# Optimization experiments

Hardware: AMD Instinct MI355X
Metric: run time of the kernel (lower is better)

## Reference

```python
import jax, jax.numpy as jnp
import numpy as np

GROUPS = 32
EPS = 1e-6


def group_norm(h, scale, bias):
    B, C, H, W = h.shape
    hg = h.reshape(B, GROUPS, -1)
    mu = hg.mean(axis=-1, keepdims=True)
    var = hg.var(axis=-1, keepdims=True)
    hg = (hg - mu) * jax.lax.rsqrt(var + EPS)
    h = hg.reshape(B, C, H, W)
    return h * scale[None, :, None, None] + bias[None, :, None, None]


def conv1x1(h, W, b):
    # 1x1 conv == per-pixel linear: (B,C,H,W) x (O,C) -> (B,O,H,W)
    return jnp.einsum('bchw,oc->bohw', h, W) + b[None, :, None, None]


def setup_inputs() -> dict:
    key = jax.random.key(0)
    ks = jax.random.split(key, 6)
    B, C, H, W = 8, 512, 64, 64
    s = 0.02
    return {
        'x': jax.random.normal(ks[0], (B, C, H, W), jnp.float32),
        'gn_scale': jnp.ones((C,), jnp.float32),
        'gn_bias': jnp.zeros((C,), jnp.float32),
        'Wq': jax.random.normal(ks[1], (C, C), jnp.float32) * s,
        'bq': jnp.zeros((C,), jnp.float32),
        'Wk': jax.random.normal(ks[2], (C, C), jnp.float32) * s,
        'bk': jnp.zeros((C,), jnp.float32),
        'Wv': jax.random.normal(ks[3], (C, C), jnp.float32) * s,
        'bv': jnp.zeros((C,), jnp.float32),
        'Wo': jax.random.normal(ks[4], (C, C), jnp.float32) * s,
        'bo': jnp.zeros((C,), jnp.float32),
    }


def reference(x, gn_scale, gn_bias, Wq, bq, Wk, bk, Wv, bv, Wo, bo):
    B, C, H, W = x.shape
    N = H * W
    h = group_norm(x, gn_scale, gn_bias)
    q = conv1x1(h, Wq, bq).reshape(B, C, N)   # (B,C,N)
    k = conv1x1(h, Wk, bk).reshape(B, C, N)
    v = conv1x1(h, Wv, bv).reshape(B, C, N)
    # scores: q^T k, scaled by C^-0.5
    w = jnp.einsum('bcq,bck->bqk', q, k) * (C ** -0.5)  # (B,N_q,N_k)
    w = jax.nn.softmax(w, axis=-1)
    # h = v @ w^T  -> (B,C,N_q)
    h = jnp.einsum('bck,bqk->bcq', v, w).reshape(B, C, H, W)
    h = conv1x1(h, Wo, bo)
    return x + h
```

## Files before the change

kernel.cpp:

```cpp
#include <hip/hip_runtime.h>
#include <math.h>

typedef __bf16 bf16_t;
typedef __bf16 bf8v __attribute__((ext_vector_type(8)));
typedef __bf16 bf4v __attribute__((ext_vector_type(4)));
typedef float  f4v  __attribute__((ext_vector_type(4)));

#define BB  8
#define CC  512
#define NN  4096
#define CPG 16
#define NCb (NN * CC)
#define WSZ (CC * CC)

#define FLG_SIZES 805306368.f
#define FLG_WS    536870912.f

__global__ void diag_out(float* out, float v) { if (threadIdx.x == 0) out[0] = v; }

__device__ __forceinline__ void gload_lds16(const bf16_t* g, bf16_t* l)
{
    __builtin_amdgcn_global_load_lds(
        (const __attribute__((address_space(1))) unsigned int*)g,
        (__attribute__((address_space(3))) unsigned int*)l, 16, 0, 0);
}

__global__ __launch_bounds__(256) void cvt_w(const float* __restrict__ a,
                                             const float* __restrict__ b,
                                             const float* __restrict__ c,
                                             const float* __restrict__ d,
                                             bf16_t* __restrict__ o)
{
    const int i = (blockIdx.x * 256 + threadIdx.x) * 4;
    const float* srcs[4] = {a, b, c, d};
#pragma unroll
    for (int m = 0; m < 4; m++) {
        float4 v = *(const float4*)(srcs[m] + i);
        bf4v w;
        w[0] = (bf16_t)v.x; w[1] = (bf16_t)v.y;
        w[2] = (bf16_t)v.z; w[3] = (bf16_t)v.w;
        *(bf4v*)(o + (size_t)m * WSZ + i) = w;
    }
}

__global__ __launch_bounds__(256) void gn_stats_part(const float* __restrict__ x,
                                                     double* __restrict__ part)
{
    const int bg = blockIdx.x >> 2;
    const int sl = blockIdx.x & 3;
    const int tid = threadIdx.x;
    const float4* xv = (const float4*)(x + (size_t)bg * CPG * NN) + sl * 4096;
    double s[4] = {0, 0, 0, 0}, ss[4] = {0, 0, 0, 0};
#pragma unroll
    for (int ii = 0; ii < 16; ii++) {
        float4 v = xv[tid + ii * 256];
        const int a = ii & 3;
        s[a]  += (double)v.x + (double)v.y + (double)v.z + (double)v.w;
        ss[a] += (double)v.x * v.x + (double)v.y * v.y
               + (double)v.z * v.z + (double)v.w * v.w;
    }
    double sT = s[0] + s[1] + s[2] + s[3];
    double ssT = ss[0] + ss[1] + ss[2] + ss[3];
    __shared__ double l1[256], l2[256];
    l1[tid] = sT; l2[tid] = ssT;
    __syncthreads();
    for (int o = 128; o > 0; o >>= 1) {
        if (tid < o) { l1[tid] += l1[tid + o]; l2[tid] += l2[tid + o]; }
        __syncthreads();
    }
    if (tid == 0) {
        part[(size_t)blockIdx.x * 2]     = l1[0];
        part[(size_t)blockIdx.x * 2 + 1] = l2[0];
    }
}

__global__ __launch_bounds__(256) void gn_stats_fin(const double* __restrict__ part,
                                                    float* __restrict__ stats)
{
    const int bg = threadIdx.x;
    double s = 0.0, ss = 0.0;
#pragma unroll
    for (int sl = 0; sl < 4; sl++) {
        s  += part[(size_t)(bg * 4 + sl) * 2];
        ss += part[(size_t)(bg * 4 + sl) * 2 + 1];
    }
    double mean = s * (1.0 / 65536.0);
    double var  = ss * (1.0 / 65536.0) - mean * mean;
    stats[bg * 2]     = (float)mean;
    stats[bg * 2 + 1] = (float)(1.0 / sqrt(var + 1e-6));
}

__global__ __launch_bounds__(256) void gn_apply_all(const float* __restrict__ x,
                                                    const float* __restrict__ gw,
                                                    const float* __restrict__ gb,
                                                    const float* __restrict__ stats,
                                                    bf16_t* __restrict__ h_all)
{
    const int b  = blockIdx.y;
    const int g  = blockIdx.x >> 4;
    const int sl = blockIdx.x & 15;
    const float* xp = x + (size_t)b * CC * NN + (size_t)g * CPG * NN;
    bf16_t* h = h_all + (size_t)b * NCb;
    const int tid = threadIdx.x;
    const float mean = stats[(b * 32 + g) * 2];
    const float rstd = stats[(b * 32 + g) * 2 + 1];
    const int cw = tid & 15;
    const float aa = rstd * gw[g * CPG + cw];
    const float bb = gb[g * CPG + cw] - mean * aa;

    __shared__ float tile[CPG][260];
    const int n0 = sl * 256;
    for (int i = tid; i < (CPG * 256) / 4; i += 256) {
        int c  = i >> 6;
        int n4 = i & 63;
        float4 v = *(const float4*)(xp + (size_t)c * NN + n0 + n4 * 4);
        tile[c][n4 * 4 + 0] = v.x;
        tile[c][n4 * 4 + 1] = v.y;
        tile[c][n4 * 4 + 2] = v.z;
        tile[c][n4 * 4 + 3] = v.w;
    }
    __syncthreads();
#pragma unroll
    for (int j = 0; j < 16; j++) {
        int n = (tid >> 4) + 16 * j;
        float v = tile[cw][n] * aa + bb;
        h[(size_t)(n0 + n) * CC + g * CPG + cw] = (bf16_t)v;
    }
}

__global__ __launch_bounds__(256) void gn_apply(const float* __restrict__ xb,
                                                const float* __restrict__ gw,
                                                const float* __restrict__ gb,
                                                const float* __restrict__ stats,
                                                bf16_t* __restrict__ h,
                                                int bg0)
{
    const int g  = blockIdx.x >> 4;
    const int sl = blockIdx.x & 15;
    const float* xp = xb + (size_t)g * CPG * NN;
    const int tid = threadIdx.x;
    const float mean = stats[(bg0 + g) * 2];
    const float rstd = stats[(bg0 + g) * 2 + 1];
    const int cw = tid & 15;
    const float aa = rstd * gw[g * CPG + cw];
    const float bb = gb[g * CPG + cw] - mean * aa;

    __shared__ float tile[CPG][260];
    const int n0 = sl * 256;
    for (int i = tid; i < (CPG * 256) / 4; i += 256) {
        int c  = i >> 6;
        int n4 = i & 63;
        float4 v = *(const float4*)(xp + (size_t)c * NN + n0 + n4 * 4);
        tile[c][n4 * 4 + 0] = v.x;
        tile[c][n4 * 4 + 1] = v.y;
        tile[c][n4 * 4 + 2] = v.z;
        tile[c][n4 * 4 + 3] = v.w;
    }
    __syncthreads();
#pragma unroll
    for (int j = 0; j < 16; j++) {
        int n = (tid >> 4) + 16 * j;
        float v = tile[cw][n] * aa + bb;
        h[(size_t)(n0 + n) * CC + g * CPG + cw] = (bf16_t)v;
    }
}

#define ABUF (128 * 32)
#define BBUF (256 * 32)
#define NBUF 3

__device__ __forceinline__ void stage_tile(
    const bf16_t* pa, const bf16_t* pb, int lda, int ldb,
    bf16_t* lA, bf16_t* lB)
{
    gload_lds16(pa,                     lA);
    gload_lds16(pa + (size_t)16 * lda,  lA + 16 * 32);
    gload_lds16(pb,                     lB);
    gload_lds16(pb + (size_t)16 * ldb,  lB + 16 * 32);
    gload_lds16(pb + (size_t)32 * ldb,  lB + 32 * 32);
    gload_lds16(pb + (size_t)48 * ldb,  lB + 48 * 32);
}

__device__ __forceinline__ void gemm_core_w(
    const bf16_t* __restrict__ A, const bf16_t* __restrict__ B,
    int K, int lda, int ldb, size_t m0, size_t n0,
    bf16_t* Asm, bf16_t* Bsm,
    int wave, int lane, int wm, int wn, int fr, int fq, f4v acc[4][8])
{
    const int gr  = lane >> 2;
    const int gcs = (((lane & 3) ^ (gr & 3)) << 3);
    const bf16_t* pa = A + (m0 + wave * 32 + gr) * lda + gcs;
    const bf16_t* pb = B + (n0 + wave * 64 + gr) * ldb + gcs;
    const int la0 = (wave * 32) * 32;
    const int lb0 = (wave * 64) * 32;
    const int fqs = ((fq ^ (fr & 3)) << 3);

    stage_tile(pa, pb, lda, ldb, Asm + la0, Bsm + lb0);
    if (K > 32)
        stage_tile(pa + 32, pb + 32, lda, ldb,
                   Asm + ABUF + la0, Bsm + BBUF + lb0);

    int buf = 0;
    for (int kt = 0; kt < K; kt += 32) {
        if (kt + 64 < K) {
            const int nb = (buf + 2 >= NBUF) ? buf + 2 - NBUF : buf + 2;
            stage_tile(pa + kt + 64, pb + kt + 64, lda, ldb,
                       Asm + nb * ABUF + la0, Bsm + nb * BBUF + lb0);
            asm volatile("s_waitcnt vmcnt(12)" ::: "memory");
        } else if (kt + 32 < K) {
            asm volatile("s_waitcnt vmcnt(6)" ::: "memory");
        } else {
            asm volatile("s_waitcnt vmcnt(0)" ::: "memory");
        }
        __builtin_amdgcn_s_barrier();

        const bf16_t* As = Asm + buf * ABUF;
        const bf16_t* Bs = Bsm + buf * BBUF;
        bf8v af[4], bfv[8];
#pragma unroll
        for (int j = 0; j < 8; j++)
            bfv[j] = *(const bf8v*)(Bs + (wn + j * 16 + fr) * 32 + fqs);
#pragma unroll
        for (int i = 0; i < 4; i++)
            af[i] = *(const bf8v*)(As + (wm + i * 16 + fr) * 32 + fqs);
#pragma unroll
        for (int i = 0; i < 4; i++)
#pragma unroll
            for (int j = 0; j < 8; j++)
                acc[i][j] = __builtin_amdgcn_mfma_f32_16x16x32_bf16(
                    af[i], bfv[j], acc[i][j], 0, 0, 0);

        __builtin_amdgcn_s_barrier();
        buf = (buf + 1 == NBUF) ? 0 : buf + 1;
    }
}

template <int MODE>
__global__ __launch_bounds__(256, 2) void gemm_bt(
    const bf16_t* __restrict__ A, const bf16_t* __restrict__ B,
    void* __restrict__ Og, const float* __restrict__ bias,
    const float* __restrict__ resid, float scale,
    int K, int lda, int ldb, int ldo)
{
    __shared__ bf16_t Asm[NBUF * ABUF];
    __shared__ bf16_t Bsm[NBUF * BBUF];
    const int tid  = threadIdx.x;
    const int lane = tid & 63, wave = tid >> 6;
    const int wm = (wave >> 1) << 6, wn = (wave & 1) << 7;
    const int fr = lane & 15, fq = lane >> 4;
    const size_t m0 = (size_t)blockIdx.x * 128, n0 = (size_t)blockIdx.y * 256;

    f4v acc[4][8];
#pragma unroll
    for (int i = 0; i < 4; i++)
#pragma unroll
        for (int j = 0; j < 8; j++) acc[i][j] = (f4v){0.f, 0.f, 0.f, 0.f};

    gemm_core_w(A, B, K, lda, ldb, m0, n0, Asm, Bsm,
                wave, lane, wm, wn, fr, fq, acc);

    if (MODE == 0) {
        bf16_t* out = (bf16_t*)Og;
#pragma unroll
        for (int i = 0; i < 4; i++) {
            const int mb = (int)m0 + wm + i * 16 + fq * 4;
#pragma unroll
            for (int j = 0; j < 8; j++) {
                const int n = (int)n0 + wn + j * 16 + fr;
                const float bn = bias ? bias[n] : 0.f;
#pragma unroll
                for (int t = 0; t < 4; t++)
                    out[(size_t)(mb + t) * ldo + n] =
                        (bf16_t)(acc[i][j][t] * scale + bn);
            }
        }
    } else {
        float* out = (float*)Og;
#pragma unroll
        for (int i = 0; i < 4; i++) {
            const int mb = (int)m0 + wm + i * 16 + fq * 4;
#pragma unroll
            for (int j = 0; j < 8; j++) {
                const int n = (int)n0 + wn + j * 16 + fr;
                const float bn = bias[n];
                float4 rq = *(const float4*)(resid + (size_t)n * ldo + mb);
                float4 o4;
                o4.x = acc[i][j][0] * scale + bn + rq.x;
                o4.y = acc[i][j][1] * scale + bn + rq.y;
                o4.z = acc[i][j][2] * scale + bn + rq.z;
                o4.w = acc[i][j][3] * scale + bn + rq.w;
                *(float4*)(out + (size_t)n * ldo + mb) = o4;
            }
        }
    }
}

__global__ __launch_bounds__(256, 2) void gemm_qkv(
    const bf16_t* __restrict__ h, const bf16_t* __restrict__ Wb,
    const float* __restrict__ bq, const float* __restrict__ bk,
    const float* __restrict__ bv,
    bf16_t* __restrict__ q, bf16_t* __restrict__ k, bf16_t* __restrict__ v)
{
    __shared__ bf16_t Asm[NBUF * ABUF];
    __shared__ bf16_t Bsm[NBUF * BBUF];
    const int z = blockIdx.z;
    const bf16_t* B = Wb + (size_t)z * WSZ;
    const float* bias = (z == 0) ? bq : (z == 1) ? bk : bv;
    bf16_t* out = (z == 0) ? q : (z == 1) ? k : v;

    const int tid  = threadIdx.x;
    const int lane = tid & 63, wave = tid >> 6;
    const int wm = (wave >> 1) << 6, wn = (wave & 1) << 7;
    const int fr = lane & 15, fq = lane >> 4;
    const size_t m0 = (size_t)blockIdx.x * 128, n0 = (size_t)blockIdx.y * 256;

    f4v acc[4][8];
#pragma unroll
    for (int i = 0; i < 4; i++)
#pragma unroll
        for (int j = 0; j < 8; j++) acc[i][j] = (f4v){0.f, 0.f, 0.f, 0.f};

    gemm_core_w(h, B, 512, 512, 512, m0, n0, Asm, Bsm,
                wave, lane, wm, wn, fr, fq, acc);

    if (z < 2) {
#pragma unroll
        for (int i = 0; i < 4; i++) {
            const int mb = (int)m0 + wm + i * 16 + fq * 4;
#pragma unroll
            for (int j = 0; j < 8; j++) {
                const int n = (int)n0 + wn + j * 16 + fr;
                const float bn = bias[n];
#pragma unroll
                for (int t = 0; t < 4; t++)
                    out[(size_t)(mb + t) * 512 + n] =
                        (bf16_t)(acc[i][j][t] + bn);
            }
        }
    } else {
#pragma unroll
        for (int i = 0; i < 4; i++) {
            const int mb = (int)m0 + wm + i * 16 + fq * 4;
#pragma unroll
            for (int j = 0; j < 8; j++) {
                const int n = (int)n0 + wn + j * 16 + fr;
                const float bn = bias[n];
                bf4v pk;
#pragma unroll
                for (int t = 0; t < 4; t++)
                    pk[t] = (bf16_t)(acc[i][j][t] + bn);
                *(bf4v*)(out + (size_t)n * NN + mb) = pk;
            }
        }
    }
}

__global__ __launch_bounds__(256, 2) void gemm_pv_split(
    const bf16_t* __restrict__ A, const bf16_t* __restrict__ B,
    float* __restrict__ P, int KS)
{
    __shared__ bf16_t Asm[NBUF * ABUF];
    __shared__ bf16_t Bsm[NBUF * BBUF];
    const int tid  = threadIdx.x;
    const int lane = tid & 63, wave = tid >> 6;
    const int wm = (wave >> 1) << 6, wn = (wave & 1) << 7;
    const int fr = lane & 15, fq = lane >> 4;
    const size_t m0 = (size_t)blockIdx.x * 128, n0 = (size_t)blockIdx.y * 256;
    const int z  = blockIdx.z;
    const int k0 = z * KS;

    f4v acc[4][8];
#pragma unroll
    for (int i = 0; i < 4; i++)
#pragma unroll
        for (int j = 0; j < 8; j++) acc[i][j] = (f4v){0.f, 0.f, 0.f, 0.f};

    gemm_core_w(A + k0, B + k0, KS, NN, NN, m0, n0, Asm, Bsm,
                wave, lane, wm, wn, fr, fq, acc);

    float* out = P + (size_t)z * NCb;
#pragma unroll
    for (int i = 0; i < 4; i++) {
        const int mb = (int)m0 + wm + i * 16 + fq * 4;
#pragma unroll
        for (int j = 0; j < 8; j++) {
            const int n = (int)n0 + wn + j * 16 + fr;
#pragma unroll
            for (int t = 0; t < 4; t++)
                out[(size_t)(mb + t) * CC + n] = acc[i][j][t];
        }
    }
}

__global__ __launch_bounds__(256) void pv_reduce(const float* __restrict__ P,
                                                 bf16_t* __restrict__ O, int NS)
{
    const size_t i = ((size_t)blockIdx.x * 256 + threadIdx.x) * 4;
    float4 s = *(const float4*)(P + i);
    for (int z = 1; z < NS; z++) {
        float4 t = *(const float4*)(P + (size_t)z * NCb + i);
        s.x += t.x; s.y += t.y; s.z += t.z; s.w += t.w;
    }
    bf4v o;
    o[0] = (bf16_t)s.x; o[1] = (bf16_t)s.y;
    o[2] = (bf16_t)s.z; o[3] = (bf16_t)s.w;
    *(bf4v*)(O + i) = o;
}

#define SL8 8192

__device__ __forceinline__ void stage_g(const bf16_t* g, int ld, bf16_t* slot,
                                        int r0, int srow, int schk)
{
    gload_lds16(g + (size_t)(r0 + srow) * ld + schk,      slot + r0 * 32);
    gload_lds16(g + (size_t)(r0 + 16 + srow) * ld + schk, slot + (r0 + 16) * 32);
}

__device__ __forceinline__ void rd4(bf8v* dst, const bf16_t* slot, int base,
                                    int fr, int rchk)
{
#pragma unroll
    for (int i = 0; i < 4; i++)
        dst[i] = *(const bf8v*)(slot + (base + i * 16 + fr) * 32 + rchk);
}

template <int IH>
__device__ __forceinline__ void mma16(const bf8v* af, const bf8v* bfv,
                                      f4v (&acc)[8][4])
{
    __builtin_amdgcn_s_setprio(1);
#pragma unroll
    for (int i = 0; i < 4; i++)
#pragma unroll
        for (int j = 0; j < 4; j++)
            acc[IH * 4 + i][j] = __builtin_amdgcn_mfma_f32_16x16x32_bf16(
                af[i], bfv[j], acc[IH * 4 + i][j], 0, 0, 0);
    __builtin_amdgcn_s_setprio(0);
}

#define FENCE8 asm volatile("" ::: "memory")
#define BAR8   do { FENCE8; __builtin_amdgcn_s_barrier(); FENCE8; } while (0)

__device__ __forceinline__ void gemm_core8(
    const bf16_t* __restrict__ A, const bf16_t* __restrict__ B,
    int K, int lda, int ldb, size_t m0, size_t n0,
    bf16_t* lds, f4v (&acc)[8][4])
{
    const int tid  = threadIdx.x;
    const int lane = tid & 63, wave = tid >> 6;
    const int wm2 = wave >> 2, wn4 = wave & 3;
    const int fr = lane & 15, fq = lane >> 4;
    const int srow = lane >> 2;
    const int schk = ((lane & 3) ^ ((srow >> 1) & 3)) << 3;
    const int r0   = wave * 32;
    const int rchk = ((fq ^ ((fr >> 1) & 3)) << 3);

    const bf16_t* Ag = A + m0 * lda;
    const bf16_t* Bg = B + n0 * ldb;
    const int NT = K >> 6;

    bf16_t* S0 = lds;
    bf16_t* S1 = lds + 1 * SL8;
    bf16_t* S2 = lds + 2 * SL8;
    bf16_t* S3 = lds + 3 * SL8;
    bf16_t* S4 = lds + 4 * SL8;
    bf16_t* S5 = lds + 5 * SL8;
    bf16_t* S6 = lds + 6 * SL8;
    bf16_t* S7 = lds + 7 * SL8;

    const int abase = wm2 * 128;
    const int bbase = wn4 * 64;

    stage_g(Ag,      lda, S0, r0, srow, schk);
    stage_g(Ag + 32, lda, S1, r0, srow, schk);
    stage_g(Bg,      ldb, S2, r0, srow, schk);
    stage_g(Bg + 32, ldb, S3, r0, srow, schk);
    stage_g(Bg + 64, ldb, S6, r0, srow, schk);
    stage_g(Ag + 64, lda, S4, r0, srow, schk);
    stage_g(Bg + 96, ldb, S7, r0, srow, schk);
    asm volatile("s_waitcnt vmcnt(6)" ::: "memory");
    __builtin_amdgcn_s_barrier();
    FENCE8;

    bf8v af[4], bfv[4];
    const int iters = NT >> 1;
    for (int it = 0; it < iters; it++) {
        const int t1k = (2 * it + 1) << 6;
        const int t2k = (2 * it + 2) << 6;
        const int t3k = (2 * it + 3) << 6;
        const bool s23 = (2 * it + 2) < NT;

        rd4(af, S0, abase, fr, rchk);
        rd4(bfv, S2, bbase, fr, rchk);
        stage_g(Ag + t1k + 32, lda, S5, r0, srow, schk);
        BAR8; mma16<0>(af, bfv, acc); BAR8;

        rd4(af, S0, abase + 64, fr, rchk);
        if (s23) stage_g(Bg + t2k, ldb, S2, r0, srow, schk);
        BAR8; mma16<1>(af, bfv, acc); BAR8;

        rd4(af, S1, abase, fr, rchk);
        rd4(bfv, S3, bbase, fr, rchk);
        if (s23) stage_g(Ag + t2k, lda, S0, r0, srow, schk);
        BAR8; mma16<0>(af, bfv, acc); BAR8;

        rd4(af, S1, abase + 64, fr, rchk);
        if (s23) {
            stage_g(Bg + t2k + 32, ldb, S3, r0, srow, schk);
            asm volatile("s_waitcnt vmcnt(6)" ::: "memory");
        } else {
            asm volatile("s_waitcnt vmcnt(0)" ::: "memory");
        }
        BAR8; mma16<1>(af, bfv, acc); BAR8;

        rd4(af, S4, abase, fr, rchk);
        rd4(bfv, S6, bbase, fr, rchk);
        if (s23) stage_g(Ag + t2k + 32, lda, S1, r0, srow, schk);
        BAR8; mma16<0>(af, bfv, acc); BAR8;

        rd4(af, S4, abase + 64, fr, rchk);
        if (s23) stage_g(Bg + t3k, ldb, S6, r0, srow, schk);
        BAR8; mma16<1>(af, bfv, acc); BAR8;

        rd4(af, S5, abase, fr, rchk);
        rd4(bfv, S7, bbase, fr, rchk);
        if (s23) stage_g(Ag + t3k, lda, S4, r0, srow, schk);
        BAR8; mma16<0>(af, bfv, acc); BAR8;

        rd4(af, S5, abase + 64, fr, rchk);
        if (s23) {
            stage_g(Bg + t3k + 32, ldb, S7, r0, srow, schk);
            asm volatile("s_waitcnt vmcnt(6)" ::: "memory");
        } else {
            asm volatile("s_waitcnt vmcnt(0)" ::: "memory");
        }
        BAR8; mma16<1>(af, bfv, acc); BAR8;
    }
}

__global__ __launch_bounds__(512, 2) void gemm_qkv_all8(
    const bf16_t* __restrict__ h_all, const bf16_t* __restrict__ Wb,
    const float* __restrict__ bq, const float* __restrict__ bk,
    const float* __restrict__ bv,
    bf16_t* __restrict__ q_all, bf16_t* __restrict__ k_all,
    bf16_t* __restrict__ v_all)
{
    __shared__ bf16_t lds8[8 * SL8];
    const int sel = blockIdx.z >> 3;
    const int b   = blockIdx.z & 7;
    const bf16_t* A = h_all + (size_t)b * NCb;
    const bf16_t* B = Wb + (size_t)sel * WSZ;
    const float* bias = (sel == 0) ? bq : (sel == 1) ? bk : bv;
    bf16_t* out = ((sel == 0) ? q_all : (sel == 1) ? k_all : v_all)
                + (size_t)b * NCb;
    const size_t m0 = (size_t)blockIdx.x * 256, n0 = (size_t)blockIdx.y * 256;

    f4v acc[8][4];
#pragma unroll
    for (int i = 0; i < 8; i++)
#pragma unroll
        for (int j = 0; j < 4; j++) acc[i][j] = (f4v){0.f, 0.f, 0.f, 0.f};

    gemm_core8(A, B, 512, 512, 512, m0, n0, lds8, acc);

    const int lane = threadIdx.x & 63, wave = threadIdx.x >> 6;
    const int wm2 = wave >> 2, wn4 = wave & 3;
    const int fr = lane & 15, fq = lane >> 4;

    if (sel < 2) {
#pragma unroll
        for (int ig = 0; ig < 8; ig++) {
            const int mb = (int)m0 + wm2 * 128 + ig * 16 + fq * 4;
#pragma unroll
            for (int j = 0; j < 4; j++) {
                const int n = (int)n0 + wn4 * 64 + j * 16 + fr;
                const float bn = bias[n];
#pragma unroll
                for (int t = 0; t < 4; t++)
                    out[(size_t)(mb + t) * 512 + n] =
                        (bf16_t)(acc[ig][j][t] + bn);
            }
        }
    } else {
#pragma unroll
        for (int ig = 0; ig < 8; ig++) {
            const int mb = (int)m0 + wm2 * 128 + ig * 16 + fq * 4;
#pragma unroll
            for (int j = 0; j < 4; j++) {
                const int n = (int)n0 + wn4 * 64 + j * 16 + fr;
                const float bn = bias[n];
                bf4v pk;
#pragma unroll
                for (int t = 0; t < 4; t++)
                    pk[t] = (bf16_t)(acc[ig][j][t] + bn);
                *(bf4v*)(out + (size_t)n * NN + mb) = pk;
            }
        }
    }
}

__global__ __launch_bounds__(512, 2) void gemm_qkt8(
    const bf16_t* __restrict__ q_all, const bf16_t* __restrict__ k_all,
    bf16_t* __restrict__ S2b, int bp, float scale)
{
    __shared__ bf16_t lds8[8 * SL8];
    const int z = blockIdx.z;
    const bf16_t* A = q_all + (size_t)(bp + z) * NCb;
    const bf16_t* B = k_all + (size_t)(bp + z) * NCb;
    bf16_t* out = S2b + (size_t)z * NN * NN;
    const size_t m0 = (size_t)blockIdx.x * 256, n0 = (size_t)blockIdx.y * 256;

    f4v acc[8][4];
#pragma unroll
    for (int i = 0; i < 8; i++)
#pragma unroll
        for (int j = 0; j < 4; j++) acc[i][j] = (f4v){0.f, 0.f, 0.f, 0.f};

    gemm_core8(A, B, 512, 512, 512, m0, n0, lds8, acc);

    const int lane = threadIdx.x & 63, wave = threadIdx.x >> 6;
    const int wm2 = wave >> 2, wn4 = wave & 3;
    const int fr = lane & 15, fq = lane >> 4;
#pragma unroll
    for (int ig = 0; ig < 8; ig++) {
        const int mb = (int)m0 + wm2 * 128 + ig * 16 + fq * 4;
#pragma unroll
        for (int j = 0; j < 4; j++) {
            const int n = (int)n0 + wn4 * 64 + j * 16 + fr;
#pragma unroll
            for (int t = 0; t < 4; t++)
                out[(size_t)(mb + t) * NN + n] = (bf16_t)(acc[ig][j][t] * scale);
        }
    }
}

__global__ __launch_bounds__(512, 2) void gemm_pv28(
    const bf16_t* __restrict__ S2b, const bf16_t* __restrict__ v_all,
    float* __restrict__ P, int bp)
{
    __shared__ bf16_t lds8[8 * SL8];
    const int slot = blockIdx.z >> 2;
    const int s    = blockIdx.z & 3;
    const int k0   = s * 1024;
    const bf16_t* A = S2b + (size_t)slot * NN * NN + k0;
    const bf16_t* B = v_all + (size_t)(bp + slot) * NCb + k0;
    float* out = P + ((size_t)slot * 4 + s) * NCb;
    const size_t m0 = (size_t)blockIdx.x * 256, n0 = (size_t)blockIdx.y * 256;

    f4v acc[8][4];
#pragma unroll
    for (int i = 0; i < 8; i++)
#pragma unroll
        for (int j = 0; j < 4; j++) acc[i][j] = (f4v){0.f, 0.f, 0.f, 0.f};

    gemm_core8(A, B, 1024, NN, NN, m0, n0, lds8, acc);

    const int lane = threadIdx.x & 63, wave = threadIdx.x >> 6;
    const int wm2 = wave >> 2, wn4 = wave & 3;
    const int fr = lane & 15, fq = lane >> 4;
#pragma unroll
    for (int ig = 0; ig < 8; ig++) {
        const int mb = (int)m0 + wm2 * 128 + ig * 16 + fq * 4;
#pragma unroll
        for (int j = 0; j < 4; j++) {
            const int n = (int)n0 + wn4 * 64 + j * 16 + fr;
#pragma unroll
            for (int t = 0; t < 4; t++)
                out[(size_t)(mb + t) * CC + n] = acc[ig][j][t];
        }
    }
}

__global__ __launch_bounds__(512, 2) void gemm_out_all8(
    const bf16_t* __restrict__ Oall, const bf16_t* __restrict__ Wo,
    float* __restrict__ outg, const float* __restrict__ bo,
    const float* __restrict__ x)
{
    __shared__ bf16_t lds8[8 * SL8];
    const int b = blockIdx.z;
    const bf16_t* A = Oall + (size_t)b * NCb;
    float* out = outg + (size_t)b * CC * NN;
    const float* resid = x + (size_t)b * CC * NN;
    const size_t m0 = (size_t)blockIdx.x * 256, n0 = (size_t)blockIdx.y * 256;

    f4v acc[8][4];
#pragma unroll
    for (int i = 0; i < 8; i++)
#pragma unroll
        for (int j = 0; j < 4; j++) acc[i][j] = (f4v){0.f, 0.f, 0.f, 0.f};

    gemm_core8(A, Wo, 512, 512, 512, m0, n0, lds8, acc);

    const int lane = threadIdx.x & 63, wave = threadIdx.x >> 6;
    const int wm2 = wave >> 2, wn4 = wave & 3;
    const int fr = lane & 15, fq = lane >> 4;
#pragma unroll
    for (int ig = 0; ig < 8; ig++) {
        const int mb = (int)m0 + wm2 * 128 + ig * 16 + fq * 4;
#pragma unroll
        for (int j = 0; j < 4; j++) {
            const int n = (int)n0 + wn4 * 64 + j * 16 + fr;
            const float bn = bo[n];
            float4 rq = *(const float4*)(resid + (size_t)n * NN + mb);
            float4 o4;
            o4.x = acc[ig][j][0] + bn + rq.x;
            o4.y = acc[ig][j][1] + bn + rq.y;
            o4.z = acc[ig][j][2] + bn + rq.z;
            o4.w = acc[ig][j][3] + bn + rq.w;
            *(float4*)(out + (size_t)n * NN + mb) = o4;
        }
    }
}

__global__ __launch_bounds__(256) void pv_reduce2(const float* __restrict__ P,
                                                  bf16_t* __restrict__ O_all,
                                                  int bp)
{
    const int slot = blockIdx.y;
    const size_t i = ((size_t)blockIdx.x * 256 + threadIdx.x) * 4;
    const float* Ps = P + (size_t)slot * 4 * NCb;
    float4 sv = *(const float4*)(Ps + i);
#pragma unroll
    for (int z = 1; z < 4; z++) {
        float4 t = *(const float4*)(Ps + (size_t)z * NCb + i);
        sv.x += t.x; sv.y += t.y; sv.z += t.z; sv.w += t.w;
    }
    bf4v o;
    o[0] = (bf16_t)sv.x; o[1] = (bf16_t)sv.y;
    o[2] = (bf16_t)sv.z; o[3] = (bf16_t)sv.w;
    *(bf4v*)(O_all + (size_t)(bp + slot) * NCb + i) = o;
}

__global__ __launch_bounds__(256) void softmax_kernel(bf16_t* __restrict__ S)
{
    const int wave = threadIdx.x >> 6, lane = threadIdx.x & 63;
    const size_t row = (size_t)blockIdx.x * 4 + wave;
    bf16_t* p = S + row * NN;
    float f[64];
    float mx = -1e30f;
#pragma unroll
    for (int c = 0; c < 8; c++) {
        bf8v v = ((const bf8v*)p)[c * 64 + lane];
#pragma unroll
        for (int j = 0; j < 8; j++) {
            f[c * 8 + j] = (float)v[j];
            mx = fmaxf(mx, f[c * 8 + j]);
        }
    }
#pragma unroll
    for (int off = 32; off > 0; off >>= 1) mx = fmaxf(mx, __shfl_xor(mx, off));
    float sum = 0.f;
#pragma unroll
    for (int i = 0; i < 64; i++) { f[i] = expf(f[i] - mx); sum += f[i]; }
#pragma unroll
    for (int off = 32; off > 0; off >>= 1) sum += __shfl_xor(sum, off);
    const float inv = 1.f / sum;
#pragma unroll
    for (int c = 0; c < 8; c++) {
        bf8v o;
#pragma unroll
        for (int j = 0; j < 8; j++) o[j] = (bf16_t)(f[c * 8 + j] * inv);
        ((bf8v*)p)[c * 64 + lane] = o;
    }
}

extern "C" void kernel_launch(void* const* d_in, const int* in_sizes, int n_in,
                              void* d_out, int out_size, void* d_ws, size_t ws_size,
                              hipStream_t stream)
{
    const float* x  = (const float*)d_in[0];
    const float* gw = (const float*)d_in[1];
    const float* gb = (const float*)d_in[2];
    const float* Wq = (const float*)d_in[3];
    const float* bq = (const float*)d_in[4];
    const float* Wk = (const float*)d_in[5];
    const float* bk = (const float*)d_in[6];
    const float* Wv = (const float*)d_in[7];
    const float* bv = (const float*)d_in[8];
    const float* Wo = (const float*)d_in[9];
    const float* bo = (const float*)d_in[10];
    float* out = (float*)d_out;

    bool ok = (n_in == 11) && (out_size == BB * CC * NN) &&
              (in_sizes[0] == BB * CC * NN) &&
              (in_sizes[1] == CC) && (in_sizes[2] == CC) &&
              (in_sizes[3] == WSZ) && (in_sizes[4] == CC) &&
              (in_sizes[5] == WSZ) && (in_sizes[6] == CC) &&
              (in_sizes[7] == WSZ) && (in_sizes[8] == CC) &&
              (in_sizes[9] == WSZ) && (in_sizes[10] == CC);
    if (!ok) { diag_out<<<dim3(1), 64, 0, stream>>>(out, FLG_SIZES); return; }

    const float sc = 0.044194173824159216f;

    bf16_t* Wb    = (bf16_t*)d_ws;
    float*  stats = (float*)(Wb + (size_t)4 * WSZ);
    double* part  = (double*)(stats + 1024);
    bf16_t* base  = (bf16_t*)(part + 2048);
    const size_t head = (size_t)4 * WSZ * 2 + 1024 * 4 + 2048 * 8;

    const size_t sfull = (size_t)NN * NN * 2;

    cvt_w<<<dim3(256), 256, 0, stream>>>(Wq, Wk, Wv, Wo, Wb);
    gn_stats_part<<<dim3(1024), 256, 0, stream>>>(x, part);
    gn_stats_fin<<<dim3(1), 256, 0, stream>>>(part, stats);

    if (ws_size >= head + (size_t)4 * BB * NCb * 2 + 2 * sfull) {
        bf16_t* h_all = base;
        bf16_t* q_all = h_all + (size_t)BB * NCb;
        bf16_t* k_all = q_all + (size_t)BB * NCb;
        bf16_t* v_all = k_all + (size_t)BB * NCb;
        bf16_t* S2    = v_all + (size_t)BB * NCb;
        float*  P     = out;
        bf16_t* O_all = h_all;

        gn_apply_all<<<dim3(512, 8), 256, 0, stream>>>(x, gw, gb, stats, h_all);
        gemm_qkv_all8<<<dim3(16, 2, 24), 512, 0, stream>>>(
            h_all, Wb, bq, bk, bv, q_all, k_all, v_all);

        for (int bp = 0; bp < BB; bp += 2) {
            gemm_qkt8<<<dim3(16, 16, 2), 512, 0, stream>>>(
                q_all, k_all, S2, bp, sc);
            softmax_kernel<<<dim3(2 * NN / 4), 256, 0, stream>>>(S2);
            gemm_pv28<<<dim3(16, 2, 8), 512, 0, stream>>>(S2, v_all, P, bp);
            pv_reduce2<<<dim3(NCb / 1024, 2), 256, 0, stream>>>(P, O_all, bp);
        }

        gemm_out_all8<<<dim3(16, 2, 8), 512, 0, stream>>>(
            O_all, Wb + (size_t)3 * WSZ, out, bo, x);
        return;
    }

    bf16_t* h = base;
    bf16_t* q = h + (size_t)NCb;
    bf16_t* k = q + (size_t)NCb;
    bf16_t* v = k + (size_t)NCb;
    bf16_t* S = v + (size_t)NCb;
    bf16_t* O = h;
    const size_t fixed = head + (size_t)4 * NCb * 2;

    if (ws_size < fixed + (size_t)128 * NN * 2) {
        diag_out<<<dim3(1), 64, 0, stream>>>(out, FLG_WS); return;
    }

    int NS = 0;
    if (ws_size >= fixed + sfull + (size_t)8 * NCb * 4)      NS = 8;
    else if (ws_size >= fixed + sfull + (size_t)4 * NCb * 4) NS = 4;
    else if (ws_size >= fixed + sfull + (size_t)2 * NCb * 4) NS = 2;

    if (NS) {
        float* P = (float*)(S + (size_t)NN * NN);
        for (int b = 0; b < BB; b++) {
            const float* xb   = x   + (size_t)b * CC * NN;
            float*       outb = out + (size_t)b * CC * NN;

            gn_apply<<<dim3(512), 256, 0, stream>>>(xb, gw, gb, stats, h, b * 32);
            gemm_qkv<<<dim3(32, 2, 3), 256, 0, stream>>>(h, Wb, bq, bk, bv, q, k, v);

            gemm_bt<0><<<dim3(32, 16), 256, 0, stream>>>(
                q, k, S, nullptr, nullptr, sc, 512, 512, 512, 4096);
            softmax_kernel<<<dim3(NN / 4), 256, 0, stream>>>(S);

            gemm_pv_split<<<dim3(32, 2, NS), 256, 0, stream>>>(S, v, P, NN / NS);
            pv_reduce<<<dim3(NCb / 1024), 256, 0, stream>>>(P, O, NS);

            gemm_bt<2><<<dim3(32, 2), 256, 0, stream>>>(
                O, Wb + (size_t)3 * WSZ, outb, bo, xb, 1.f,
                512, 512, 512, 4096);
        }
        return;
    }

    int CH = 128;
    while (CH < NN && fixed + (size_t)(CH * 2) * NN * 2 <= ws_size) CH *= 2;

    for (int b = 0; b < BB; b++) {
        const float* xb   = x   + (size_t)b * CC * NN;
        float*       outb = out + (size_t)b * CC * NN;

        gn_apply<<<dim3(512), 256, 0, stream>>>(xb, gw, gb, stats, h, b * 32);
        gemm_qkv<<<dim3(32, 2, 3), 256, 0, stream>>>(h, Wb, bq, bk, bv, q, k, v);

        for (int r0 = 0; r0 < NN; r0 += CH) {
            gemm_bt<0><<<dim3(CH / 128, 16), 256, 0, stream>>>(
                q + (size_t)r0 * CC, k, S, nullptr, nullptr, sc,
                512, 512, 512, 4096);
            softmax_kernel<<<dim3(CH / 4), 256, 0, stream>>>(S);
            gemm_bt<0><<<dim3(CH / 128, 2), 256, 0, stream>>>(
                S, v, O + (size_t)r0 * CC, nullptr, nullptr, 1.f,
                4096, 4096, 4096, 512);
        }

        gemm_bt<2><<<dim3(32, 2), 256, 0, stream>>>(
            O, Wb + (size_t)3 * WSZ, outb, bo, xb, 1.f,
            512, 512, 512, 4096);
    }
}
```

Baseline: 757.0 us.

## Process four batches per attention pass and split PV over two K halves

Adds a new path, used when the workspace is large enough, that materializes score matrices for four batches at once instead of two. This halves the number of QK^T/softmax/PV/reduce launch rounds. The PV GEMM now splits K into two halves rather than four, which lowers the partial-sum traffic in the reduce step. In exchange the workspace must hold twice as many NxN bf16 score buffers, and each PV block does a longer K loop.

```diff
diff --git a/kernel.cpp b/kernel.cpp
--- a/kernel.cpp
+++ b/kernel.cpp
@@ -671,6 +671,43 @@
     }
 }
 
+__global__ __launch_bounds__(512, 2) void gemm_pv28q(
+    const bf16_t* __restrict__ S4b, const bf16_t* __restrict__ v_all,
+    float* __restrict__ P, int bp)
+{
+    __shared__ bf16_t lds8[8 * SL8];
+    const int slot = blockIdx.z >> 1;
+    const int s    = blockIdx.z & 1;
+    const int k0   = s * 2048;
+    const bf16_t* A = S4b + (size_t)slot * NN * NN + k0;
+    const bf16_t* B = v_all + (size_t)(bp + slot) * NCb + k0;
+    float* out = P + ((size_t)slot * 2 + s) * NCb;
+    const size_t m0 = (size_t)blockIdx.x * 256, n0 = (size_t)blockIdx.y * 256;
+
+    f4v acc[8][4];
+#pragma unroll
+    for (int i = 0; i < 8; i++)
+#pragma unroll
+        for (int j = 0; j < 4; j++) acc[i][j] = (f4v){0.f, 0.f, 0.f, 0.f};
+
+    gemm_core8(A, B, 2048, NN, NN, m0, n0, lds8, acc);
+
+    const int lane = threadIdx.x & 63, wave = threadIdx.x >> 6;
+    const int wm2 = wave >> 2, wn4 = wave & 3;
+    const int fr = lane & 15, fq = lane >> 4;
+#pragma unroll
+    for (int ig = 0; ig < 8; ig++) {
+        const int mb = (int)m0 + wm2 * 128 + ig * 16 + fq * 4;
+#pragma unroll
+        for (int j = 0; j < 4; j++) {
+            const int n = (int)n0 + wn4 * 64 + j * 16 + fr;
+#pragma unroll
+            for (int t = 0; t < 4; t++)
+                out[(size_t)(mb + t) * CC + n] = acc[ig][j][t];
+        }
+    }
+}
+
 __global__ __launch_bounds__(512, 2) void gemm_out_all8(
     const bf16_t* __restrict__ Oall, const bf16_t* __restrict__ Wo,
     float* __restrict__ outg, const float* __restrict__ bo,
@@ -728,6 +765,21 @@
     bf4v o;
     o[0] = (bf16_t)sv.x; o[1] = (bf16_t)sv.y;
     o[2] = (bf16_t)sv.z; o[3] = (bf16_t)sv.w;
+    *(bf4v*)(O_all + (size_t)(bp + slot) * NCb + i) = o;
+}
+
+__global__ __launch_bounds__(256) void pv_reduce2q(const float* __restrict__ P,
+                                                   bf16_t* __restrict__ O_all,
+                                                   int bp)
+{
+    const int slot = blockIdx.y;
+    const size_t i = ((size_t)blockIdx.x * 256 + threadIdx.x) * 4;
+    const float* Ps = P + (size_t)slot * 2 * NCb;
+    float4 a = *(const float4*)(Ps + i);
+    float4 b = *(const float4*)(Ps + (size_t)NCb + i);
+    bf4v o;
+    o[0] = (bf16_t)(a.x + b.x); o[1] = (bf16_t)(a.y + b.y);
+    o[2] = (bf16_t)(a.z + b.z); o[3] = (bf16_t)(a.w + b.w);
     *(bf4v*)(O_all + (size_t)(bp + slot) * NCb + i) = o;
 }
 
@@ -804,6 +856,32 @@
     gn_stats_part<<<dim3(1024), 256, 0, stream>>>(x, part);
     gn_stats_fin<<<dim3(1), 256, 0, stream>>>(part, stats);
 
+    if (ws_size >= head + (size_t)4 * BB * NCb * 2 + 4 * sfull) {
+        bf16_t* h_all = base;
+        bf16_t* q_all = h_all + (size_t)BB * NCb;
+        bf16_t* k_all = q_all + (size_t)BB * NCb;
+        bf16_t* v_all = k_all + (size_t)BB * NCb;
+        bf16_t* S4    = v_all + (size_t)BB * NCb;
+        float*  P     = out;
+        bf16_t* O_all = h_all;
+
+        gn_apply_all<<<dim3(512, 8), 256, 0, stream>>>(x, gw, gb, stats, h_all);
+        gemm_qkv_all8<<<dim3(16, 2, 24), 512, 0, stream>>>(
+            h_all, Wb, bq, bk, bv, q_all, k_all, v_all);
+
+        for (int bp = 0; bp < BB; bp += 4) {
+            gemm_qkt8<<<dim3(16, 16, 4), 512, 0, stream>>>(
+                q_all, k_all, S4, bp, sc);
+            softmax_kernel<<<dim3(4 * NN / 4), 256, 0, stream>>>(S4);
+            gemm_pv28q<<<dim3(16, 2, 8), 512, 0, stream>>>(S4, v_all, P, bp);
+            pv_reduce2q<<<dim3(NCb / 1024, 4), 256, 0, stream>>>(P, O_all, bp);
+        }
+
+        gemm_out_all8<<<dim3(16, 2, 8), 512, 0, stream>>>(
+            O_all, Wb + (size_t)3 * WSZ, out, bo, x);
+        return;
+    }
+
     if (ws_size >= head + (size_t)4 * BB * NCb * 2 + 2 * sfull) {
         bf16_t* h_all = base;
         bf16_t* q_all = h_all + (size_t)BB * NCb;
```

Measured after the change: 728.5 us. 1.04x faster.
